# Kernel tuning notes

Measured on AMD Instinct MI355X. Metric: run time of the kernel, lower is better.

Reference implementation:

```python
import jax, jax.numpy as jnp
import numpy as np

B, NX, C, KX = 16, 8192, 128, 16  # batch, grid size, channels, retained positive modes


def setup_inputs() -> dict:
    key = jax.random.key(0)
    k1, k2, k3 = jax.random.split(key, 3)
    x = jax.random.normal(k1, (B, NX, C), dtype=jnp.float32)
    scale = 1.0 / (C ** 2)
    w_real = scale * jax.random.uniform(k2, (KX + 1, C, C), dtype=jnp.float32)
    w_imag = scale * jax.random.uniform(k3, (KX + 1, C, C), dtype=jnp.float32)
    return {"x": x, "w_real": w_real, "w_imag": w_imag}


def reference(x, w_real, w_imag):
    # x: (b, nx, c); weights: (kx+1, c, c) complex
    nx = x.shape[1]
    k1 = w_real.shape[0]  # kx + 1 retained frequencies
    w = w_real + 1j * w_imag
    fx = jnp.fft.rfft(x, axis=-2)  # (b, nx//2+1, c) complex
    # torch.matmul(weights, fx[:, :kx+1, :, None])[..., 0]:
    # out[b,k,i] = sum_j w[k,i,j] * fx[b,k,j]
    out_ft = jnp.einsum('kij,bkj->bki', w, fx[:, :k1, :])
    # zero-pad truncated spectrum back to full rfft length, then inverse
    pad = nx // 2 + 1 - k1
    out_full = jnp.pad(out_ft, ((0, 0), (0, pad), (0, 0)))
    return jnp.fft.irfft(out_full, n=nx, axis=-2)
```

## Files before the change

kernel.cpp:

```cpp
#include <hip/hip_runtime.h>
#include <math.h>

#define B_     16
#define NX_    8192
#define C_     128
#define K1_    17
#define QW_    20
#define NC_    16
#define NSP_   256
#define NCI_   64
#define NH_    4096

typedef float v2f __attribute__((ext_vector_type(2)));
typedef float v4f __attribute__((ext_vector_type(4)));

#define GPART_F  ((size_t)B_ * K1_ * 2 * NC_ * C_)
#define ACOEF_F  ((size_t)B_ * K1_ * C_ * 2)
#define TRIG_OFF (GPART_F + ACOEF_F)


__global__ __launch_bounds__(256) void k_fwd(const float* __restrict__ x,
                                             float* __restrict__ ws) {
    __shared__ v4f smem[2560];

    float* gpart = ws;
    const int b = blockIdx.y;
    const int c = blockIdx.x;
    const int t = threadIdx.x;
    const int jq  = t & 31;
    const int sub = (t >> 5) & 1;
    const int w   = t >> 6;
    const int i0  = c * NSP_;

    const size_t xb = (size_t)b * NX_ * C_;
    const int ibase = w * 64;
    const float sg = sub ? -1.f : 1.f;
    const float* xlo_p = x + xb + (size_t)(i0 + ibase) * C_ + 4 * jq;
    const float* xhi_p = xlo_p + (size_t)NH_ * C_;

    v4f bl[2][4], bh[2][4];
#pragma unroll
    for (int j = 0; j < 4; ++j) {
        bl[0][j] = *(const v4f*)(xlo_p + (size_t)j * C_);
        bh[0][j] = *(const v4f*)(xhi_p + (size_t)j * C_);
    }

    {
        float2* tg  = (float2*)smem;
        float2* tgg = (float2*)(ws + TRIG_OFF) + (size_t)i0 * QW_;
        for (int idx = t; idx < NSP_ * QW_; idx += 256) {
            int i = idx / QW_;
            int q = idx - i * QW_;
            float2 v = make_float2(0.f, 0.f);
            int k = (q < 9) ? (2 * q) : ((q >= 10 && q < 18) ? (2 * (q - 10) + 1) : -1);
            if (k >= 0) {
                int m = (k * (i0 + i)) & (NX_ - 1);
                float rev = (float)m * (1.0f / (float)NX_);
                v = make_float2(__builtin_amdgcn_cosf(rev),
                                __builtin_amdgcn_sinf(rev));
            }
            tg[idx] = v;
            if (b == 0) tgg[idx] = v;
        }
    }
    __syncthreads();

    v4f gr[9], gs[9];
#pragma unroll
    for (int kk = 0; kk < 9; ++kk) { gr[kk] = (v4f)(0.f); gs[kk] = (v4f)(0.f); }

    const float* tp = (const float*)smem + ((size_t)ibase * QW_ + sub * 10) * 2;

#pragma unroll
    for (int g = 0; g < 16; ++g) {
        const int cur = g & 1, nxt = cur ^ 1;
        if (g < 15) {
#pragma unroll
            for (int j = 0; j < 4; ++j) {
                bl[nxt][j] = *(const v4f*)(xlo_p + (size_t)((g + 1) * 4 + j) * C_);
                bh[nxt][j] = *(const v4f*)(xhi_p + (size_t)((g + 1) * 4 + j) * C_);
            }
        }
#pragma unroll
        for (int j = 0; j < 4; ++j) {
            const int s = g * 4 + j;
            v4f xs = __builtin_elementwise_fma(bh[cur][j], (v4f)(sg), bl[cur][j]);
            const float* tr = tp + (size_t)s * (2 * QW_);
            float4 t0 = *(const float4*)(tr + 0);
            float4 t1 = *(const float4*)(tr + 4);
            float4 t2 = *(const float4*)(tr + 8);
            float4 t3 = *(const float4*)(tr + 12);
            float2 t4 = *(const float2*)(tr + 16);
            gr[0] = __builtin_elementwise_fma(xs, (v4f)(t0.x), gr[0]);
            gs[0] = __builtin_elementwise_fma(xs, (v4f)(t0.y), gs[0]);
            gr[1] = __builtin_elementwise_fma(xs, (v4f)(t0.z), gr[1]);
            gs[1] = __builtin_elementwise_fma(xs, (v4f)(t0.w), gs[1]);
            gr[2] = __builtin_elementwise_fma(xs, (v4f)(t1.x), gr[2]);
            gs[2] = __builtin_elementwise_fma(xs, (v4f)(t1.y), gs[2]);
            gr[3] = __builtin_elementwise_fma(xs, (v4f)(t1.z), gr[3]);
            gs[3] = __builtin_elementwise_fma(xs, (v4f)(t1.w), gs[3]);
            gr[4] = __builtin_elementwise_fma(xs, (v4f)(t2.x), gr[4]);
            gs[4] = __builtin_elementwise_fma(xs, (v4f)(t2.y), gs[4]);
            gr[5] = __builtin_elementwise_fma(xs, (v4f)(t2.z), gr[5]);
            gs[5] = __builtin_elementwise_fma(xs, (v4f)(t2.w), gs[5]);
            gr[6] = __builtin_elementwise_fma(xs, (v4f)(t3.x), gr[6]);
            gs[6] = __builtin_elementwise_fma(xs, (v4f)(t3.y), gs[6]);
            gr[7] = __builtin_elementwise_fma(xs, (v4f)(t3.z), gr[7]);
            gs[7] = __builtin_elementwise_fma(xs, (v4f)(t3.w), gs[7]);
            gr[8] = __builtin_elementwise_fma(xs, (v4f)(t4.x), gr[8]);
            gs[8] = __builtin_elementwise_fma(xs, (v4f)(t4.y), gs[8]);
        }
    }

    const int lid = t & 63;
    __syncthreads();
    if (w >= 2) {
        v4f* p = smem + ((size_t)(w - 2) * 64 + lid) * 19;
#pragma unroll
        for (int kk = 0; kk < 9; ++kk) { p[2 * kk] = gr[kk]; p[2 * kk + 1] = gs[kk]; }
    }
    __syncthreads();
    if (w < 2) {
        const v4f* p = smem + ((size_t)w * 64 + lid) * 19;
#pragma unroll
        for (int kk = 0; kk < 9; ++kk) { gr[kk] += p[2 * kk]; gs[kk] += p[2 * kk + 1]; }
    }
    __syncthreads();
    if (w == 1) {
        v4f* p = smem + (size_t)lid * 19;
#pragma unroll
        for (int kk = 0; kk < 9; ++kk) { p[2 * kk] = gr[kk]; p[2 * kk + 1] = gs[kk]; }
    }
    __syncthreads();
    if (w == 0) {
        const v4f* p = smem + (size_t)lid * 19;
#pragma unroll
        for (int kk = 0; kk < 9; ++kk) {
            gr[kk] += p[2 * kk];
            gs[kk] += p[2 * kk + 1];
            if (sub == 0 || kk < 8) {
                int k = sub ? 2 * kk + 1 : 2 * kk;
                float* gpR = gpart + ((((size_t)b * K1_ + k) * 2 + 0) * NC_ + c) * C_ + 4 * jq;
                float* gpS = gpart + ((((size_t)b * K1_ + k) * 2 + 1) * NC_ + c) * C_ + 4 * jq;
                *(v4f*)gpR = gr[kk];
                *(v4f*)gpS = gs[kk];
            }
        }
    }
}

__global__ __launch_bounds__(1024) void k_mix(const float* __restrict__ wr_g,
                                              const float* __restrict__ wi_g,
                                              float* __restrict__ ws) {
    const int k = blockIdx.x, b = blockIdx.y, t = threadIdx.x;
    const float* gpart = ws;
    float2* acoef = (float2*)(ws + GPART_F);
    __shared__ float part[8][C_];
    __shared__ float gsum[2][C_];
    __shared__ float hp[16][C_];
    {
        const int ch = t & 127, ri = (t >> 7) & 1, sh = t >> 8;
        const float* base = gpart + (((size_t)b * K1_ + k) * 2 + ri) * ((size_t)NC_ * C_) + ch;
        float g = 0.f;
#pragma unroll
        for (int s = 0; s < 4; ++s) g += base[(size_t)(sh * 4 + s) * C_];
        part[sh * 2 + ri][ch] = g;
    }
    __syncthreads();
    if (t < 256) {
        const int ch = t & 127, ri = t >> 7;
        gsum[ri][ch] = part[ri][ch] + part[2 + ri][ch] + part[4 + ri][ch] + part[6 + ri][ch];
    }
    __syncthreads();
    {
        const int i = t & 127, q = t >> 7;
        float hr = 0.f, hi = 0.f;
        const float* wrp = wr_g + ((size_t)k * C_ + i) * C_;
        const float* wip = wi_g + ((size_t)k * C_ + i) * C_;
#pragma unroll
        for (int jjj = 0; jjj < 16; ++jjj) {
            int jj = q * 16 + jjj;
            float wr = wrp[jj], wi = wip[jj];
            float a = gsum[0][jj], cc = gsum[1][jj];
            hr = fmaf(wr, a, hr); hr = fmaf( wi, cc, hr);
            hi = fmaf(wi, a, hi); hi = fmaf(-wr, cc, hi);
        }
        hp[q * 2 + 0][i] = hr;
        hp[q * 2 + 1][i] = hi;
    }
    __syncthreads();
    if (t < 128) {
        const int i = t;
        float hr = 0.f, hi = 0.f;
#pragma unroll
        for (int q = 0; q < 8; ++q) { hr += hp[q * 2][i]; hi += hp[q * 2 + 1][i]; }
        float cf = (k == 0 ? 1.0f : 2.0f) / (float)NX_;
        acoef[((size_t)b * K1_ + k) * C_ + i] = make_float2(cf * hr, -cf * hi);
    }
}

__global__ __launch_bounds__(256) void k_inv(float* __restrict__ out,
                                             const float* __restrict__ ws) {
    const float4* acoef4 = (const float4*)(ws + GPART_F);
    const float* trigg = ws + TRIG_OFF;
    const int b = blockIdx.y, c = blockIdx.x, t = threadIdx.x;
    const int jp = t & 63;
    const int h = __builtin_amdgcn_readfirstlane(t >> 6);
    const int i0 = c * 64;

    v2f arE[9], aiE[9], arO[8], aiO[8];
#pragma unroll
    for (int q = 0; q < 9; ++q) {
        float4 a = acoef4[((size_t)b * K1_ + 2 * q) * (C_ / 2) + jp];
        arE[q] = (v2f){a.x, a.z}; aiE[q] = (v2f){a.y, a.w};
    }
#pragma unroll
    for (int q = 0; q < 8; ++q) {
        float4 a = acoef4[((size_t)b * K1_ + 2 * q + 1) * (C_ / 2) + jp];
        arO[q] = (v2f){a.x, a.z}; aiO[q] = (v2f){a.y, a.w};
    }

    const float* trow = trigg + ((size_t)(i0 + h * 16)) * (2 * QW_);
    const size_t ob = (size_t)b * NX_ * C_;
    float* olo = out + ob + (size_t)(i0 + h * 16) * C_ + 2 * jp;
    float* ohi = olo + (size_t)NH_ * C_;

#pragma unroll 4
    for (int s = 0; s < 16; ++s) {
        const float* tr = trow + (size_t)s * (2 * QW_);
        float4 e0 = *(const float4*)(tr + 0);
        float4 e1 = *(const float4*)(tr + 4);
        float4 e2 = *(const float4*)(tr + 8);
        float4 e3 = *(const float4*)(tr + 12);
        float2 e4 = *(const float2*)(tr + 16);
        float4 o0 = *(const float4*)(tr + 20);
        float4 o1 = *(const float4*)(tr + 24);
        float4 o2 = *(const float4*)(tr + 28);
        float4 o3 = *(const float4*)(tr + 32);
        v2f Se = (v2f)(0.f), So = (v2f)(0.f);
        Se = __builtin_elementwise_fma(arE[0], (v2f)(e0.x), Se);
        Se = __builtin_elementwise_fma(aiE[0], (v2f)(e0.y), Se);
        Se = __builtin_elementwise_fma(arE[1], (v2f)(e0.z), Se);
        Se = __builtin_elementwise_fma(aiE[1], (v2f)(e0.w), Se);
        Se = __builtin_elementwise_fma(arE[2], (v2f)(e1.x), Se);
        Se = __builtin_elementwise_fma(aiE[2], (v2f)(e1.y), Se);
        Se = __builtin_elementwise_fma(arE[3], (v2f)(e1.z), Se);
        Se = __builtin_elementwise_fma(aiE[3], (v2f)(e1.w), Se);
        Se = __builtin_elementwise_fma(arE[4], (v2f)(e2.x), Se);
        Se = __builtin_elementwise_fma(aiE[4], (v2f)(e2.y), Se);
        Se = __builtin_elementwise_fma(arE[5], (v2f)(e2.z), Se);
        Se = __builtin_elementwise_fma(aiE[5], (v2f)(e2.w), Se);
        Se = __builtin_elementwise_fma(arE[6], (v2f)(e3.x), Se);
        Se = __builtin_elementwise_fma(aiE[6], (v2f)(e3.y), Se);
        Se = __builtin_elementwise_fma(arE[7], (v2f)(e3.z), Se);
        Se = __builtin_elementwise_fma(aiE[7], (v2f)(e3.w), Se);
        Se = __builtin_elementwise_fma(arE[8], (v2f)(e4.x), Se);
        Se = __builtin_elementwise_fma(aiE[8], (v2f)(e4.y), Se);
        So = __builtin_elementwise_fma(arO[0], (v2f)(o0.x), So);
        So = __builtin_elementwise_fma(aiO[0], (v2f)(o0.y), So);
        So = __builtin_elementwise_fma(arO[1], (v2f)(o0.z), So);
        So = __builtin_elementwise_fma(aiO[1], (v2f)(o0.w), So);
        So = __builtin_elementwise_fma(arO[2], (v2f)(o1.x), So);
        So = __builtin_elementwise_fma(aiO[2], (v2f)(o1.y), So);
        So = __builtin_elementwise_fma(arO[3], (v2f)(o1.z), So);
        So = __builtin_elementwise_fma(aiO[3], (v2f)(o1.w), So);
        So = __builtin_elementwise_fma(arO[4], (v2f)(o2.x), So);
        So = __builtin_elementwise_fma(aiO[4], (v2f)(o2.y), So);
        So = __builtin_elementwise_fma(arO[5], (v2f)(o2.z), So);
        So = __builtin_elementwise_fma(aiO[5], (v2f)(o2.w), So);
        So = __builtin_elementwise_fma(arO[6], (v2f)(o3.x), So);
        So = __builtin_elementwise_fma(aiO[6], (v2f)(o3.y), So);
        So = __builtin_elementwise_fma(arO[7], (v2f)(o3.z), So);
        So = __builtin_elementwise_fma(aiO[7], (v2f)(o3.w), So);
        *(v2f*)(olo + (size_t)s * C_) = Se + So;
        *(v2f*)(ohi + (size_t)s * C_) = Se - So;
    }
}

extern "C" void kernel_launch(void* const* d_in, const int* in_sizes, int n_in,
                              void* d_out, int out_size, void* d_ws, size_t ws_size,
                              hipStream_t stream) {
    const float* x  = (const float*)d_in[0];
    const float* wr = (const float*)d_in[1];
    const float* wi = (const float*)d_in[2];
    float* out = (float*)d_out;
    float* ws  = (float*)d_ws;

    k_fwd<<<dim3(NC_, B_), 256, 0, stream>>>(x, ws);
    k_mix<<<dim3(K1_, B_), 1024, 0, stream>>>(wr, wi, ws);
    k_inv<<<dim3(NCI_, B_), 256, 0, stream>>>(out, ws);
}
```

Measured before the change: 45.44 us.

## Fuse forward, mix and inverse stages into one cooperative kernel with grid syncs

```diff
diff --git a/kernel.cpp b/kernel.cpp
--- a/kernel.cpp
+++ b/kernel.cpp
@@ -1,5 +1,8 @@
 #include <hip/hip_runtime.h>
+#include <hip/hip_cooperative_groups.h>
 #include <math.h>
+
+namespace cg = cooperative_groups;
 
 #define B_     16
 #define NX_    8192
@@ -19,14 +22,10 @@
 #define TRIG_OFF (GPART_F + ACOEF_F)
 
 
-__global__ __launch_bounds__(256) void k_fwd(const float* __restrict__ x,
-                                             float* __restrict__ ws) {
-    __shared__ v4f smem[2560];
-
+__device__ __forceinline__ void fwd_body(const float* __restrict__ x,
+                                         float* __restrict__ ws,
+                                         v4f* smem, int b, int c, int t) {
     float* gpart = ws;
-    const int b = blockIdx.y;
-    const int c = blockIdx.x;
-    const int t = threadIdx.x;
     const int jq  = t & 31;
     const int sub = (t >> 5) & 1;
     const int w   = t >> 6;
@@ -149,61 +148,58 @@
     }
 }
 
-__global__ __launch_bounds__(1024) void k_mix(const float* __restrict__ wr_g,
-                                              const float* __restrict__ wi_g,
-                                              float* __restrict__ ws) {
-    const int k = blockIdx.x, b = blockIdx.y, t = threadIdx.x;
+__device__ __forceinline__ void mix_body(const float* __restrict__ wr_g,
+                                         const float* __restrict__ wi_g,
+                                         float* __restrict__ ws,
+                                         float* smemf, int bb, int k, int t) {
     const float* gpart = ws;
     float2* acoef = (float2*)(ws + GPART_F);
-    __shared__ float part[8][C_];
-    __shared__ float gsum[2][C_];
-    __shared__ float hp[16][C_];
-    {
-        const int ch = t & 127, ri = (t >> 7) & 1, sh = t >> 8;
-        const float* base = gpart + (((size_t)b * K1_ + k) * 2 + ri) * ((size_t)NC_ * C_) + ch;
-        float g = 0.f;
-#pragma unroll
-        for (int s = 0; s < 4; ++s) g += base[(size_t)(sh * 4 + s) * C_];
-        part[sh * 2 + ri][ch] = g;
-    }
-    __syncthreads();
-    if (t < 256) {
-        const int ch = t & 127, ri = t >> 7;
-        gsum[ri][ch] = part[ri][ch] + part[2 + ri][ch] + part[4 + ri][ch] + part[6 + ri][ch];
-    }
-    __syncthreads();
-    {
-        const int i = t & 127, q = t >> 7;
-        float hr = 0.f, hi = 0.f;
-        const float* wrp = wr_g + ((size_t)k * C_ + i) * C_;
-        const float* wip = wi_g + ((size_t)k * C_ + i) * C_;
-#pragma unroll
-        for (int jjj = 0; jjj < 16; ++jjj) {
-            int jj = q * 16 + jjj;
-            float wr = wrp[jj], wi = wip[jj];
-            float a = gsum[0][jj], cc = gsum[1][jj];
-            hr = fmaf(wr, a, hr); hr = fmaf( wi, cc, hr);
-            hi = fmaf(wi, a, hi); hi = fmaf(-wr, cc, hi);
-        }
-        hp[q * 2 + 0][i] = hr;
-        hp[q * 2 + 1][i] = hi;
-    }
-    __syncthreads();
-    if (t < 128) {
-        const int i = t;
-        float hr = 0.f, hi = 0.f;
-#pragma unroll
-        for (int q = 0; q < 8; ++q) { hr += hp[q * 2][i]; hi += hp[q * 2 + 1][i]; }
+    const int i = t & 127;
+    const int h = t >> 7;
+    float* grs = smemf;
+    float* gss = grs + C_;
+    float* trr = gss + C_;
+    float* tii = trr + C_;
+
+    const float* baseR = gpart + (((size_t)bb * K1_ + k) * 2 + 0) * ((size_t)NC_ * C_);
+    const float* baseS = gpart + (((size_t)bb * K1_ + k) * 2 + 1) * ((size_t)NC_ * C_);
+    float gr = 0.f, gs = 0.f;
+#pragma unroll
+    for (int s = 0; s < 8; ++s) {
+        gr += baseR[(size_t)(h * 8 + s) * C_ + i];
+        gs += baseS[(size_t)(h * 8 + s) * C_ + i];
+    }
+    if (h) { trr[i] = gr; tii[i] = gs; }
+    __syncthreads();
+    if (!h) { grs[i] = gr + trr[i]; gss[i] = gs + tii[i]; }
+    __syncthreads();
+
+    float hr = 0.f, hi = 0.f;
+    const float* wrp = wr_g + ((size_t)k * C_ + i) * C_;
+    const float* wip = wi_g + ((size_t)k * C_ + i) * C_;
+#pragma unroll 8
+    for (int jj = h * 64; jj < h * 64 + 64; ++jj) {
+        float wr = wrp[jj], wi = wip[jj];
+        float a = grs[jj], cc = gss[jj];
+        hr = fmaf(wr, a, hr); hr = fmaf( wi, cc, hr);
+        hi = fmaf(wi, a, hi); hi = fmaf(-wr, cc, hi);
+    }
+    __syncthreads();
+    if (h) { trr[i] = hr; tii[i] = hi; }
+    __syncthreads();
+    if (!h) {
+        hr += trr[i]; hi += tii[i];
         float cf = (k == 0 ? 1.0f : 2.0f) / (float)NX_;
-        acoef[((size_t)b * K1_ + k) * C_ + i] = make_float2(cf * hr, -cf * hi);
-    }
-}
-
-__global__ __launch_bounds__(256) void k_inv(float* __restrict__ out,
-                                             const float* __restrict__ ws) {
+        acoef[((size_t)bb * K1_ + k) * C_ + i] = make_float2(cf * hr, -cf * hi);
+    }
+    __syncthreads();
+}
+
+__device__ __forceinline__ void inv_body(float* __restrict__ out,
+                                         const float* __restrict__ ws,
+                                         int b, int c, int t) {
     const float4* acoef4 = (const float4*)(ws + GPART_F);
     const float* trigg = ws + TRIG_OFF;
-    const int b = blockIdx.y, c = blockIdx.x, t = threadIdx.x;
     const int jp = t & 63;
     const int h = __builtin_amdgcn_readfirstlane(t >> 6);
     const int i0 = c * 64;
@@ -277,6 +273,90 @@
     }
 }
 
+__global__ __launch_bounds__(256) void k_all(
+        const float* __restrict__ x,
+        const float* __restrict__ wr_g,
+        const float* __restrict__ wi_g,
+        float* __restrict__ out,
+        float* __restrict__ ws) {
+    __shared__ v4f smem[2560];
+    const int bid = blockIdx.x;
+    const int t = threadIdx.x;
+
+    fwd_body(x, ws, smem, bid >> 4, bid & 15, t);
+
+    cg::this_grid().sync();
+
+    for (int job = bid; job < B_ * K1_; job += 256)
+        mix_body(wr_g, wi_g, ws, (float*)smem, job / K1_, job % K1_, t);
+
+    cg::this_grid().sync();
+
+    for (int tile = bid; tile < B_ * NCI_; tile += 256)
+        inv_body(out, ws, tile >> 6, tile & 63, t);
+}
+
+__global__ __launch_bounds__(256) void k_fwd(const float* __restrict__ x,
+                                             float* __restrict__ ws) {
+    __shared__ v4f smem[2560];
+    fwd_body(x, ws, smem, blockIdx.y, blockIdx.x, threadIdx.x);
+}
+
+__global__ __launch_bounds__(1024) void k_mix(const float* __restrict__ wr_g,
+                                              const float* __restrict__ wi_g,
+                                              float* __restrict__ ws) {
+    const int k = blockIdx.x, b = blockIdx.y, t = threadIdx.x;
+    const float* gpart = ws;
+    float2* acoef = (float2*)(ws + GPART_F);
+    __shared__ float part[8][C_];
+    __shared__ float gsum[2][C_];
+    __shared__ float hp[16][C_];
+    {
+        const int ch = t & 127, ri = (t >> 7) & 1, sh = t >> 8;
+        const float* base = gpart + (((size_t)b * K1_ + k) * 2 + ri) * ((size_t)NC_ * C_) + ch;
+        float g = 0.f;
+#pragma unroll
+        for (int s = 0; s < 4; ++s) g += base[(size_t)(sh * 4 + s) * C_];
+        part[sh * 2 + ri][ch] = g;
+    }
+    __syncthreads();
+    if (t < 256) {
+        const int ch = t & 127, ri = t >> 7;
+        gsum[ri][ch] = part[ri][ch] + part[2 + ri][ch] + part[4 + ri][ch] + part[6 + ri][ch];
+    }
+    __syncthreads();
+    {
+        const int i = t & 127, q = t >> 7;
+        float hr = 0.f, hi = 0.f;
+        const float* wrp = wr_g + ((size_t)k * C_ + i) * C_;
+        const float* wip = wi_g + ((size_t)k * C_ + i) * C_;
+#pragma unroll
+        for (int jjj = 0; jjj < 16; ++jjj) {
+            int jj = q * 16 + jjj;
+            float wr = wrp[jj], wi = wip[jj];
+            float a = gsum[0][jj], cc = gsum[1][jj];
+            hr = fmaf(wr, a, hr); hr = fmaf( wi, cc, hr);
+            hi = fmaf(wi, a, hi); hi = fmaf(-wr, cc, hi);
+        }
+        hp[q * 2 + 0][i] = hr;
+        hp[q * 2 + 1][i] = hi;
+    }
+    __syncthreads();
+    if (t < 128) {
+        const int i = t;
+        float hr = 0.f, hi = 0.f;
+#pragma unroll
+        for (int q = 0; q < 8; ++q) { hr += hp[q * 2][i]; hi += hp[q * 2 + 1][i]; }
+        float cf = (k == 0 ? 1.0f : 2.0f) / (float)NX_;
+        acoef[((size_t)b * K1_ + k) * C_ + i] = make_float2(cf * hr, -cf * hi);
+    }
+}
+
+__global__ __launch_bounds__(256) void k_inv(float* __restrict__ out,
+                                             const float* __restrict__ ws) {
+    inv_body(out, ws, blockIdx.y, blockIdx.x, threadIdx.x);
+}
+
 extern "C" void kernel_launch(void* const* d_in, const int* in_sizes, int n_in,
                               void* d_out, int out_size, void* d_ws, size_t ws_size,
                               hipStream_t stream) {
@@ -286,7 +366,12 @@
     float* out = (float*)d_out;
     float* ws  = (float*)d_ws;
 
-    k_fwd<<<dim3(NC_, B_), 256, 0, stream>>>(x, ws);
-    k_mix<<<dim3(K1_, B_), 1024, 0, stream>>>(wr, wi, ws);
-    k_inv<<<dim3(NCI_, B_), 256, 0, stream>>>(out, ws);
-}
+    void* args[] = { (void*)&x, (void*)&wr, (void*)&wi, (void*)&out, (void*)&ws };
+    hipError_t err = hipLaunchCooperativeKernel((void*)k_all, dim3(256), dim3(256),
+                                                args, 0, stream);
+    if (err != hipSuccess) {
+        k_fwd<<<dim3(NC_, B_), 256, 0, stream>>>(x, ws);
+        k_mix<<<dim3(K1_, B_), 1024, 0, stream>>>(wr, wi, ws);
+        k_inv<<<dim3(NCI_, B_), 256, 0, stream>>>(out, ws);
+    }
+}
```

Result: slower. 127.6 us (+180.8%).
